# Performance work log

Hardware: AMD Instinct MI355X
Metric: run time of the kernel (lower is better)

## Reference

```python
import jax, jax.numpy as jnp
import numpy as np

TAU = 2.0        # spikingjelly LIFNode default tau
VTH = 1.0        # v_threshold
ALPHA = 2.0      # ATan surrogate alpha
NUM_HEADS = 8
N_WIN = 8
TOPK = 4


@jax.custom_vjp
def atan_heaviside(x):
    # spike = H(v - v_th), with ATan surrogate gradient
    return (x >= 0.0).astype(x.dtype)

def _ah_fwd(x):
    return atan_heaviside(x), x

def _ah_bwd(x, g):
    half_pi_alpha = np.float32(np.pi / 2.0 * ALPHA)
    return (g * (ALPHA / 2.0) / (1.0 + (half_pi_alpha * x) ** 2),)

atan_heaviside.defvjp(_ah_fwd, _ah_bwd)


def lif(x):
    """Multi-step LIF over leading time dim. decay_input=True, v_reset=0, detach_reset."""
    def step(v, xt):
        v = v + (xt - v) / TAU                      # charge
        s = atan_heaviside(v - VTH)                 # fire
        v = v * (1.0 - jax.lax.stop_gradient(s))    # hard reset (detached)
        return v, s
    _, spikes = jax.lax.scan(step, jnp.zeros_like(x[0]), x)
    return spikes


def setup_inputs() -> dict:
    key = jax.random.key(0)
    k1, k2, k3, k4, k5 = jax.random.split(key, 5)
    T, B, L, C = 4, 4, 1024, 256
    x = jax.random.normal(k1, (T, B, L, C), dtype=jnp.float32)
    w_qkv = jax.random.normal(k2, (C, 3 * C), dtype=jnp.float32) * (C ** -0.5)
    b_qkv = jax.random.normal(k3, (3 * C,), dtype=jnp.float32) * 0.02
    w_proj = jax.random.normal(k4, (C, C), dtype=jnp.float32) * (C ** -0.5)
    b_proj = jax.random.normal(k5, (C,), dtype=jnp.float32) * 0.02
    return {"x": x, "w_qkv": w_qkv, "b_qkv": b_qkv, "w_proj": w_proj, "b_proj": b_proj}


def reference(x, w_qkv, b_qkv, w_proj, b_proj):
    T, B, L, C = x.shape
    hd = C // NUM_HEADS
    win = L // N_WIN
    scale = hd ** -0.5

    # --- region-level routing (on raw input summed over time) ---
    xs = x.sum(axis=0).reshape(B, N_WIN, win, C)
    region = xs.sum(axis=2)                                  # [B, n_win, C]
    attn_r = jnp.einsum('bnc,bmc->bnm', region, region) * (C ** -0.5)
    _, idx = jax.lax.top_k(attn_r, TOPK)                     # [B, n_win, topk] int32

    # --- qkv + LIF spiking ---
    qkv = x @ w_qkv + b_qkv                                  # [T,B,L,3C]
    q, k, v = jnp.split(qkv, 3, axis=-1)
    q, k, v = lif(q), lif(k), lif(v)
    q = q.reshape(T, B, N_WIN, win, NUM_HEADS, hd)
    k = k.reshape(T, B, N_WIN, win, NUM_HEADS, hd)
    v = v.reshape(T, B, N_WIN, win, NUM_HEADS, hd)

    # --- gather routed KV windows (vectorized; topk-major concat like torch.cat) ---
    b_idx = jnp.arange(B)[:, None, None]                     # [B,1,1]
    k_g = k[:, b_idx, idx].reshape(T, B, N_WIN, TOPK * win, NUM_HEADS, hd)
    v_g = v[:, b_idx, idx].reshape(T, B, N_WIN, TOPK * win, NUM_HEADS, hd)

    # --- windowed attention over gathered keys ---
    attn = jnp.einsum('tbnqhd,tbnkhd->tbnhqk', q, k_g) * scale
    attn = jax.nn.softmax(attn, axis=-1)
    out = jnp.einsum('tbnhqk,tbnkhd->tbnqhd', attn, v_g).reshape(T, B, L, C)

    out = lif(out @ w_proj + b_proj)
    return out
```

## Files before the change

kernel.cpp:

```cpp
#include <hip/hip_runtime.h>
#include <cstdint>
#include <cstddef>

#define TT 4
#define BB 4
#define LL 1024
#define CC 256
#define HH 8
#define HD 32
#define NWIN 8
#define WIN 128
#define TOPKN 4
#define C3 768

__global__ __launch_bounds__(64) void region_kernel(const float* __restrict__ x,
                                                    float* __restrict__ region) {
    int bn = blockIdx.x;
    int b = bn >> 3, n = bn & 7;
    int c = blockIdx.y * 64 + threadIdx.x;
    float tot = 0.0f;
    for (int r = 0; r < WIN; ++r) {
        int l = n * WIN + r;
        float s = 0.0f;
        for (int t = 0; t < TT; ++t) {
            s += x[(((size_t)t * BB + b) * LL + l) * CC + c];
        }
        tot += s;
    }
    region[(size_t)bn * CC + c] = tot;
}

__global__ __launch_bounds__(64) void route_kernel(const float* __restrict__ region,
                                                   int* __restrict__ idx) {
    int b = blockIdx.x;
    __shared__ float reg[NWIN][CC];
    __shared__ float attn_r[NWIN][NWIN];
    int tid = threadIdx.x;
    for (int e = tid; e < NWIN * CC; e += 64)
        reg[e >> 8][e & 255] = region[(size_t)b * NWIN * CC + e];
    __syncthreads();
    int n = tid >> 3, m = tid & 7;
    float s = 0.0f;
    for (int c = 0; c < CC; ++c) s += reg[n][c] * reg[m][c];
    attn_r[n][m] = s * 0.0625f;
    __syncthreads();
    if (tid < NWIN) {
        float vals[NWIN];
        for (int m2 = 0; m2 < NWIN; ++m2) vals[m2] = attn_r[tid][m2];
        for (int kk = 0; kk < TOPKN; ++kk) {
            int bi = 0; float bv = vals[0];
            for (int m2 = 1; m2 < NWIN; ++m2) {
                if (vals[m2] > bv) { bv = vals[m2]; bi = m2; }
            }
            idx[(b * NWIN + tid) * TOPKN + kk] = bi;
            vals[bi] = -INFINITY;
        }
    }
}

__global__ __launch_bounds__(256, 3) void gemm_bias128(const float* __restrict__ A,
                                                       const float* __restrict__ W,
                                                       const float* __restrict__ bias,
                                                       float* __restrict__ C,
                                                       int M, int N, int K) {
    const int BM = 128, BN = 128, BK = 16, TM = 8;
    __shared__ float As[BK][BM + 4];
    __shared__ float Bs[BK][136];
    int tid = threadIdx.x;
    int tx = tid & 15, ty = tid >> 4;
    int bm = blockIdx.x * BM, bn = blockIdx.y * BN;
    float acc[TM][8] = {};
    for (int k0 = 0; k0 < K; k0 += BK) {
#pragma unroll
        for (int it = 0; it < 2; ++it) {
            int i = it * 256 + tid;
            int row = i >> 2, kc = (i & 3) * 4;
            float4 v = *(const float4*)(A + (size_t)(bm + row) * K + k0 + kc);
            As[kc + 0][row] = v.x; As[kc + 1][row] = v.y;
            As[kc + 2][row] = v.z; As[kc + 3][row] = v.w;
        }
#pragma unroll
        for (int it = 0; it < 2; ++it) {
            int i = it * 256 + tid;
            int kr = i >> 5, nc = (i & 31) * 4;
            float4 v = *(const float4*)(W + (size_t)(k0 + kr) * N + bn + nc);
            *(float4*)&Bs[kr][nc] = v;
        }
        __syncthreads();
#pragma unroll
        for (int kk = 0; kk < BK; ++kk) {
            float a[TM], bb[8];
            const float4* ap = (const float4*)&As[kk][ty * TM];
            float4 a0 = ap[0], a1 = ap[1];
            a[0]=a0.x; a[1]=a0.y; a[2]=a0.z; a[3]=a0.w;
            a[4]=a1.x; a[5]=a1.y; a[6]=a1.z; a[7]=a1.w;
            float4 b0 = *(const float4*)&Bs[kk][tx * 4];
            float4 b1 = *(const float4*)&Bs[kk][64 + tx * 4];
            bb[0]=b0.x; bb[1]=b0.y; bb[2]=b0.z; bb[3]=b0.w;
            bb[4]=b1.x; bb[5]=b1.y; bb[6]=b1.z; bb[7]=b1.w;
#pragma unroll
            for (int i = 0; i < TM; ++i)
#pragma unroll
                for (int j = 0; j < 8; ++j)
                    acc[i][j] = fmaf(a[i], bb[j], acc[i][j]);
        }
        __syncthreads();
    }
#pragma unroll
    for (int i = 0; i < TM; ++i) {
        int row = bm + ty * TM + i;
        int col0 = bn + tx * 4;
        int col1 = bn + 64 + tx * 4;
        float4 o0 = make_float4(acc[i][0] + bias[col0 + 0], acc[i][1] + bias[col0 + 1],
                                acc[i][2] + bias[col0 + 2], acc[i][3] + bias[col0 + 3]);
        float4 o1 = make_float4(acc[i][4] + bias[col1 + 0], acc[i][5] + bias[col1 + 1],
                                acc[i][6] + bias[col1 + 2], acc[i][7] + bias[col1 + 3]);
        *(float4*)&C[(size_t)row * N + col0] = o0;
        *(float4*)&C[(size_t)row * N + col1] = o1;
    }
}

__global__ __launch_bounds__(256, 4) void gemm_bias64(const float* __restrict__ A,
                                                      const float* __restrict__ W,
                                                      const float* __restrict__ bias,
                                                      float* __restrict__ C,
                                                      int M, int N, int K) {
    const int BM = 64, BN = 64, BK = 16;
    __shared__ float As[BK][BM + 4];
    __shared__ float Bs[BK][72];
    int tid = threadIdx.x;
    int tx = tid & 15, ty = tid >> 4;
    int bm = blockIdx.x * BM, bn = blockIdx.y * BN;
    float acc[4][4] = {};
    for (int k0 = 0; k0 < K; k0 += BK) {
        {
            int row = tid >> 2, kc = (tid & 3) * 4;
            float4 v = *(const float4*)(A + (size_t)(bm + row) * K + k0 + kc);
            As[kc + 0][row] = v.x; As[kc + 1][row] = v.y;
            As[kc + 2][row] = v.z; As[kc + 3][row] = v.w;
        }
        {
            int kr = tid >> 4, nc = (tid & 15) * 4;
            float4 v = *(const float4*)(W + (size_t)(k0 + kr) * N + bn + nc);
            *(float4*)&Bs[kr][nc] = v;
        }
        __syncthreads();
#pragma unroll
        for (int kk = 0; kk < BK; ++kk) {
            float4 av = *(const float4*)&As[kk][ty * 4];
            float4 bv = *(const float4*)&Bs[kk][tx * 4];
            float a[4] = {av.x, av.y, av.z, av.w};
            float bb[4] = {bv.x, bv.y, bv.z, bv.w};
#pragma unroll
            for (int i = 0; i < 4; ++i)
#pragma unroll
                for (int j = 0; j < 4; ++j)
                    acc[i][j] = fmaf(a[i], bb[j], acc[i][j]);
        }
        __syncthreads();
    }
#pragma unroll
    for (int i = 0; i < 4; ++i) {
        int row = bm + ty * 4 + i;
        int col = bn + tx * 4;
        float4 o = make_float4(acc[i][0] + bias[col + 0], acc[i][1] + bias[col + 1],
                               acc[i][2] + bias[col + 2], acc[i][3] + bias[col + 3]);
        *(float4*)&C[(size_t)row * N + col] = o;
    }
}

__global__ __launch_bounds__(256) void lif_kernel(const float* src, float* dst, size_t stride) {
    size_t i = ((size_t)blockIdx.x * blockDim.x + threadIdx.x) * 4;
    float v[4] = {0.f, 0.f, 0.f, 0.f};
    for (int t = 0; t < TT; ++t) {
        float4 xv4 = *(const float4*)(src + (size_t)t * stride + i);
        float xv[4] = {xv4.x, xv4.y, xv4.z, xv4.w};
        float sp[4];
#pragma unroll
        for (int j = 0; j < 4; ++j) {
            v[j] = v[j] + (xv[j] - v[j]) * 0.5f;
            bool fire = (v[j] >= 1.0f);
            sp[j] = fire ? 1.0f : 0.0f;
            v[j] = fire ? 0.0f : v[j];
        }
        *(float4*)(dst + (size_t)t * stride + i) = make_float4(sp[0], sp[1], sp[2], sp[3]);
    }
}

__global__ __launch_bounds__(256) void pack_kernel(const float* __restrict__ spk,
                                                   uint32_t* __restrict__ pk) {
    size_t g = (size_t)blockIdx.x * 256 + threadIdx.x;
    int row = (int)(g >> 9);
    int col = (int)(g & 511);
    float v = spk[(size_t)row * C3 + col];
    unsigned long long m = __ballot(v >= 0.5f);
    int lane = threadIdx.x & 63;
    if ((lane & 31) == 0)
        pk[(size_t)row * 16 + (col >> 5)] = (lane < 32) ? (uint32_t)m : (uint32_t)(m >> 32);
}

__global__ __launch_bounds__(256, 4) void attn_fused(const float* __restrict__ spk,
                                                     const uint32_t* __restrict__ pk,
                                                     const int* __restrict__ idxws,
                                                     float* __restrict__ out) {
    int bid = blockIdx.x;
    int h = bid & 1, hp = (bid >> 1) & 3, n = (bid >> 3) & 7, b = (bid >> 6) & 3, t = bid >> 8;
    __shared__ __align__(16) float Vlds[2][64][32];
    __shared__ float ptab[33][WIN];
    __shared__ __align__(16) uint32_t kbs[4 * WIN];
    int tid = threadIdx.x;
    int q = tid & 127, dh = tid >> 7;
    int lbase = (t * BB + b) * LL;

    const int* ip = idxws + (b * NWIN + n) * TOPKN;
    int s0r = ip[0], s1r = ip[1], s2r = ip[2], s3r = ip[3];

#pragma unroll 2
    for (int e = tid; e < 512; e += 256) {
        int w = e >> 7;
        int sw = (w == 0) ? s0r : (w == 1) ? s1r : (w == 2) ? s2r : s3r;
        int row = sw * WIN + (e & 127);
        kbs[e] = pk[(size_t)(lbase + row) * 16 + 8 + hp * 2 + h];
    }
    uint32_t qw = pk[(size_t)(lbase + n * WIN + q) * 16 + hp * 2 + h];
    __syncthreads();

    const float* vsrc = spk + (size_t)lbase * C3 + 512 + hp * 64 + h * 32
                        + (size_t)(tid >> 3) * C3 + (tid & 7) * 4;
    int wvoff = (tid >> 6) * 1024;

#define STAGE_HALF(hw_)                                                              \
    do {                                                                             \
        int hw = (hw_);                                                              \
        int ww = hw >> 1;                                                            \
        int sw = (ww == 0) ? s0r : (ww == 1) ? s1r : (ww == 2) ? s2r : s3r;          \
        const float* src = vsrc + (size_t)sw * (WIN * C3)                            \
                                + (size_t)(hw & 1) * 64 * C3;                        \
        char* lb = (char*)(&Vlds[hw & 1][0][0]) + wvoff;                             \
        __builtin_amdgcn_global_load_lds(                                            \
            (const __attribute__((address_space(1))) void*)src,                      \
            (__attribute__((address_space(3))) void*)lb, 16, 0, 0);                  \
        __builtin_amdgcn_global_load_lds(                                            \
            (const __attribute__((address_space(1))) void*)(src + 32 * C3),          \
            (__attribute__((address_space(3))) void*)(lb + 4096), 16, 0, 0);         \
    } while (0)

    STAGE_HALF(0);
    STAGE_HALF(1);

    const float ALPHA_SC = 0.17677669529663687f;
    const uint4* kb4 = (const uint4*)kbs;
    if (tid < 128) {
        int smax = 0;
#pragma unroll 8
        for (int k4 = 0; k4 < 128; ++k4) {
            uint4 w4 = kb4[k4];
            smax = max(smax, __popc(qw & w4.x));
            smax = max(smax, __popc(qw & w4.y));
            smax = max(smax, __popc(qw & w4.z));
            smax = max(smax, __popc(qw & w4.w));
        }
        float am = __fmul_rn((float)smax, ALPHA_SC);
        float Z = 0.0f;
#pragma unroll 4
        for (int k4 = 0; k4 < 128; ++k4) {
            uint4 w4 = kb4[k4];
            Z += expf(__fsub_rn(__fmul_rn((float)__popc(qw & w4.x), ALPHA_SC), am));
            Z += expf(__fsub_rn(__fmul_rn((float)__popc(qw & w4.y), ALPHA_SC), am));
            Z += expf(__fsub_rn(__fmul_rn((float)__popc(qw & w4.z), ALPHA_SC), am));
            Z += expf(__fsub_rn(__fmul_rn((float)__popc(qw & w4.w), ALPHA_SC), am));
        }
        for (int s = 0; s <= 32; ++s)
            ptab[s][tid] = expf(__fsub_rn(__fmul_rn((float)s, ALPHA_SC), am)) / Z;
    }

    float acc[16];
#pragma unroll
    for (int d = 0; d < 16; ++d) acc[d] = 0.0f;

    asm volatile("s_waitcnt vmcnt(2)" ::: "memory");
    __syncthreads();

#pragma unroll
    for (int hw = 0; hw < 8; ++hw) {
        const uint4* kw4 = kb4 + hw * 16;
        const float* vb = &Vlds[hw & 1][0][dh * 16];
#pragma unroll 2
        for (int g = 0; g < 16; ++g) {
            uint4 kw = kw4[g];
            const float* pr = vb + g * 128;
#pragma unroll
            for (int jp = 0; jp < 2; ++jp) {
                uint32_t ka = (jp == 0) ? kw.x : kw.z;
                uint32_t kb_ = (jp == 0) ? kw.y : kw.w;
                float Pa = ptab[__popc(qw & ka)][q];
                float Pb = ptab[__popc(qw & kb_)][q];
                const float4* va = (const float4*)(pr + jp * 64);
                const float4* vbp = (const float4*)(pr + jp * 64 + 32);
                float4 a0 = va[0], a1 = va[1], a2 = va[2], a3 = va[3];
                float4 b0 = vbp[0], b1 = vbp[1], b2 = vbp[2], b3 = vbp[3];
                acc[ 0] = fmaf(Pa, a0.x, acc[ 0]);
                acc[ 1] = fmaf(Pa, a0.y, acc[ 1]);
                acc[ 2] = fmaf(Pa, a0.z, acc[ 2]);
                acc[ 3] = fmaf(Pa, a0.w, acc[ 3]);
                acc[ 4] = fmaf(Pa, a1.x, acc[ 4]);
                acc[ 5] = fmaf(Pa, a1.y, acc[ 5]);
                acc[ 6] = fmaf(Pa, a1.z, acc[ 6]);
                acc[ 7] = fmaf(Pa, a1.w, acc[ 7]);
                acc[ 8] = fmaf(Pa, a2.x, acc[ 8]);
                acc[ 9] = fmaf(Pa, a2.y, acc[ 9]);
                acc[10] = fmaf(Pa, a2.z, acc[10]);
                acc[11] = fmaf(Pa, a2.w, acc[11]);
                acc[12] = fmaf(Pa, a3.x, acc[12]);
                acc[13] = fmaf(Pa, a3.y, acc[13]);
                acc[14] = fmaf(Pa, a3.z, acc[14]);
                acc[15] = fmaf(Pa, a3.w, acc[15]);
                acc[ 0] = fmaf(Pb, b0.x, acc[ 0]);
                acc[ 1] = fmaf(Pb, b0.y, acc[ 1]);
                acc[ 2] = fmaf(Pb, b0.z, acc[ 2]);
                acc[ 3] = fmaf(Pb, b0.w, acc[ 3]);
                acc[ 4] = fmaf(Pb, b1.x, acc[ 4]);
                acc[ 5] = fmaf(Pb, b1.y, acc[ 5]);
                acc[ 6] = fmaf(Pb, b1.z, acc[ 6]);
                acc[ 7] = fmaf(Pb, b1.w, acc[ 7]);
                acc[ 8] = fmaf(Pb, b2.x, acc[ 8]);
                acc[ 9] = fmaf(Pb, b2.y, acc[ 9]);
                acc[10] = fmaf(Pb, b2.z, acc[10]);
                acc[11] = fmaf(Pb, b2.w, acc[11]);
                acc[12] = fmaf(Pb, b3.x, acc[12]);
                acc[13] = fmaf(Pb, b3.y, acc[13]);
                acc[14] = fmaf(Pb, b3.z, acc[14]);
                acc[15] = fmaf(Pb, b3.w, acc[15]);
            }
        }

        if (hw < 7) {
            __syncthreads();
            if (hw < 6) {
                STAGE_HALF(hw + 2);
                asm volatile("s_waitcnt vmcnt(2)" ::: "memory");
            } else {
                asm volatile("s_waitcnt vmcnt(0)" ::: "memory");
            }
            __syncthreads();
        }
    }
#undef STAGE_HALF

    size_t ob = (size_t)(lbase + n * WIN + q) * CC + (hp * 2 + h) * 32 + dh * 16;
#pragma unroll
    for (int d = 0; d < 16; ++d) out[ob + d] = acc[d];
}

extern "C" void kernel_launch(void* const* d_in, const int* in_sizes, int n_in,
                              void* d_out, int out_size, void* d_ws, size_t ws_size,
                              hipStream_t stream) {
    const float* x      = (const float*)d_in[0];
    const float* w_qkv  = (const float*)d_in[1];
    const float* b_qkv  = (const float*)d_in[2];
    const float* w_proj = (const float*)d_in[3];
    const float* b_proj = (const float*)d_in[4];
    float* ws = (float*)d_ws;

    float* qkv      = ws;
    float* attn_out = ws + 12582912;
    float* proj     = ws + 16777216;
    uint32_t* pkb   = (uint32_t*)proj;
    float* region   = ws + 20971520;
    int*   idxp     = (int*)(ws + 20979712);
    float* outp     = (float*)d_out;

    region_kernel<<<dim3(BB * NWIN, 4), dim3(64), 0, stream>>>(x, region);
    route_kernel<<<dim3(BB), dim3(64), 0, stream>>>(region, idxp);
    gemm_bias128<<<dim3(128, 6), dim3(256), 0, stream>>>(x, w_qkv, b_qkv, qkv,
                                                         TT * BB * LL, C3, CC);
    lif_kernel<<<dim3(3072), dim3(256), 0, stream>>>(qkv, qkv, (size_t)BB * LL * C3);
    pack_kernel<<<dim3(32768), dim3(256), 0, stream>>>(qkv, pkb);
    attn_fused<<<dim3(TT * BB * NWIN * 4 * 2), dim3(256), 0, stream>>>(qkv, pkb, idxp, attn_out);
    gemm_bias64<<<dim3(256, 4), dim3(256), 0, stream>>>(attn_out, w_proj, b_proj, proj,
                                                        TT * BB * LL, CC, CC);
    lif_kernel<<<dim3(1024), dim3(256), 0, stream>>>(proj, outp, (size_t)BB * LL * CC);
}
```

Before: 280.9 us.

## Fuse LIF with bit packing and split softmax stats from PV attention

Replaces the separate LIF and pack kernels with one kernel that runs LIF over time, writes float spikes only for V, and packs q/k spikes into bitmasks via ballots. Softmax max and normalizer computation moves to a separate attn_sm kernel, so the PV kernel no longer has half its threads idle during the stats pass. The PV kernel now computes two queries per thread over 8 dims each to reuse V LDS loads, and stores with vector writes. This adds one kernel launch and a small workspace buffer, and uses a permuted bit order inside the packed words that stays consistent between q and k.

```diff
diff --git a/kernel.cpp b/kernel.cpp
--- a/kernel.cpp
+++ b/kernel.cpp
@@ -187,29 +187,105 @@
     }
 }
 
-__global__ __launch_bounds__(256) void pack_kernel(const float* __restrict__ spk,
-                                                   uint32_t* __restrict__ pk) {
-    size_t g = (size_t)blockIdx.x * 256 + threadIdx.x;
-    int row = (int)(g >> 9);
-    int col = (int)(g & 511);
-    float v = spk[(size_t)row * C3 + col];
-    unsigned long long m = __ballot(v >= 0.5f);
-    int lane = threadIdx.x & 63;
-    if ((lane & 31) == 0)
-        pk[(size_t)row * 16 + (col >> 5)] = (lane < 32) ? (uint32_t)m : (uint32_t)(m >> 32);
-}
-
-__global__ __launch_bounds__(256, 4) void attn_fused(const float* __restrict__ spk,
-                                                     const uint32_t* __restrict__ pk,
-                                                     const int* __restrict__ idxws,
-                                                     float* __restrict__ out) {
+__global__ __launch_bounds__(192) void lif_pack_kernel(float* __restrict__ qkv,
+                                                       uint32_t* __restrict__ pk) {
+    int row = blockIdx.x;
+    int tid = threadIdx.x;
+    int c = tid * 4;
+    int wid = tid >> 6;
+    int lane = tid & 63;
+    const size_t stride = (size_t)BB * LL * C3;
+    float* base = qkv + (size_t)row * C3 + c;
+
+    float v[4] = {0.f, 0.f, 0.f, 0.f};
+    for (int t = 0; t < TT; ++t) {
+        float4 xv4 = *(const float4*)(base + (size_t)t * stride);
+        float xv[4] = {xv4.x, xv4.y, xv4.z, xv4.w};
+        bool fire[4];
+        float sp[4];
+#pragma unroll
+        for (int j = 0; j < 4; ++j) {
+            v[j] = v[j] + (xv[j] - v[j]) * 0.5f;
+            fire[j] = (v[j] >= 1.0f);
+            sp[j] = fire[j] ? 1.0f : 0.0f;
+            v[j] = fire[j] ? 0.0f : v[j];
+        }
+        if (c >= 512)
+            *(float4*)(base + (size_t)t * stride) = make_float4(sp[0], sp[1], sp[2], sp[3]);
+        unsigned long long B0 = __ballot(fire[0]);
+        unsigned long long B1 = __ballot(fire[1]);
+        unsigned long long B2 = __ballot(fire[2]);
+        unsigned long long B3 = __ballot(fire[3]);
+        if (lane < 8 && wid < 2) {
+            uint32_t word = ((uint32_t)(B0 >> (8 * lane)) & 0xFFu)
+                          | (((uint32_t)(B1 >> (8 * lane)) & 0xFFu) << 8)
+                          | (((uint32_t)(B2 >> (8 * lane)) & 0xFFu) << 16)
+                          | (((uint32_t)(B3 >> (8 * lane)) & 0xFFu) << 24);
+            pk[((size_t)t * BB * LL + row) * 16 + wid * 8 + lane] = word;
+        }
+    }
+}
+
+__global__ __launch_bounds__(256) void attn_sm(const uint32_t* __restrict__ pk,
+                                               const int* __restrict__ idxws,
+                                               float2* __restrict__ amz) {
+    int bid = blockIdx.x;
+    int hp = bid & 3, n = (bid >> 2) & 7, b = (bid >> 5) & 3, t = bid >> 7;
+    __shared__ uint32_t kbs[2][512];
+    int tid = threadIdx.x;
+    int q = tid & 127, h = tid >> 7;
+    int lbase = (t * BB + b) * LL;
+
+    const int* ip = idxws + (b * NWIN + n) * TOPKN;
+    int s0r = ip[0], s1r = ip[1], s2r = ip[2], s3r = ip[3];
+
+#pragma unroll 4
+    for (int e = tid; e < 1024; e += 256) {
+        int hh = e >> 9, kk = e & 511;
+        int w = kk >> 7;
+        int sw = (w == 0) ? s0r : (w == 1) ? s1r : (w == 2) ? s2r : s3r;
+        int row = sw * WIN + (kk & 127);
+        kbs[hh][kk] = pk[(size_t)(lbase + row) * 16 + 8 + hp * 2 + hh];
+    }
+    uint32_t qw = pk[(size_t)(lbase + n * WIN + q) * 16 + hp * 2 + h];
+    __syncthreads();
+
+    const float ALPHA_SC = 0.17677669529663687f;
+    const uint4* kb4 = (const uint4*)kbs[h];
+    int smax = 0;
+#pragma unroll 8
+    for (int k4 = 0; k4 < 128; ++k4) {
+        uint4 w4 = kb4[k4];
+        smax = max(smax, __popc(qw & w4.x));
+        smax = max(smax, __popc(qw & w4.y));
+        smax = max(smax, __popc(qw & w4.z));
+        smax = max(smax, __popc(qw & w4.w));
+    }
+    float am = __fmul_rn((float)smax, ALPHA_SC);
+    float Z = 0.0f;
+#pragma unroll 4
+    for (int k4 = 0; k4 < 128; ++k4) {
+        uint4 w4 = kb4[k4];
+        Z += expf(__fsub_rn(__fmul_rn((float)__popc(qw & w4.x), ALPHA_SC), am));
+        Z += expf(__fsub_rn(__fmul_rn((float)__popc(qw & w4.y), ALPHA_SC), am));
+        Z += expf(__fsub_rn(__fmul_rn((float)__popc(qw & w4.z), ALPHA_SC), am));
+        Z += expf(__fsub_rn(__fmul_rn((float)__popc(qw & w4.w), ALPHA_SC), am));
+    }
+    amz[(size_t)(lbase + n * WIN + q) * HH + hp * 2 + h] = make_float2(am, Z);
+}
+
+__global__ __launch_bounds__(256, 4) void attn_pv(const float* __restrict__ spk,
+                                                  const uint32_t* __restrict__ pk,
+                                                  const int* __restrict__ idxws,
+                                                  const float2* __restrict__ amz,
+                                                  float* __restrict__ out) {
     int bid = blockIdx.x;
     int h = bid & 1, hp = (bid >> 1) & 3, n = (bid >> 3) & 7, b = (bid >> 6) & 3, t = bid >> 8;
     __shared__ __align__(16) float Vlds[2][64][32];
     __shared__ float ptab[33][WIN];
     __shared__ __align__(16) uint32_t kbs[4 * WIN];
     int tid = threadIdx.x;
-    int q = tid & 127, dh = tid >> 7;
+    int qg = tid & 63, dh = tid >> 6;
     int lbase = (t * BB + b) * LL;
 
     const int* ip = idxws + (b * NWIN + n) * TOPKN;
@@ -222,8 +298,8 @@
         int row = sw * WIN + (e & 127);
         kbs[e] = pk[(size_t)(lbase + row) * 16 + 8 + hp * 2 + h];
     }
-    uint32_t qw = pk[(size_t)(lbase + n * WIN + q) * 16 + hp * 2 + h];
-    __syncthreads();
+    uint32_t qw0 = pk[(size_t)(lbase + n * WIN + qg) * 16 + hp * 2 + h];
+    uint32_t qw1 = pk[(size_t)(lbase + n * WIN + qg + 64) * 16 + hp * 2 + h];
 
     const float* vsrc = spk + (size_t)lbase * C3 + 512 + hp * 64 + h * 32
                         + (size_t)(tid >> 3) * C3 + (tid & 7) * 4;
@@ -248,43 +324,28 @@
     STAGE_HALF(0);
     STAGE_HALF(1);
 
-    const float ALPHA_SC = 0.17677669529663687f;
-    const uint4* kb4 = (const uint4*)kbs;
-    if (tid < 128) {
-        int smax = 0;
-#pragma unroll 8
-        for (int k4 = 0; k4 < 128; ++k4) {
-            uint4 w4 = kb4[k4];
-            smax = max(smax, __popc(qw & w4.x));
-            smax = max(smax, __popc(qw & w4.y));
-            smax = max(smax, __popc(qw & w4.z));
-            smax = max(smax, __popc(qw & w4.w));
-        }
-        float am = __fmul_rn((float)smax, ALPHA_SC);
-        float Z = 0.0f;
-#pragma unroll 4
-        for (int k4 = 0; k4 < 128; ++k4) {
-            uint4 w4 = kb4[k4];
-            Z += expf(__fsub_rn(__fmul_rn((float)__popc(qw & w4.x), ALPHA_SC), am));
-            Z += expf(__fsub_rn(__fmul_rn((float)__popc(qw & w4.y), ALPHA_SC), am));
-            Z += expf(__fsub_rn(__fmul_rn((float)__popc(qw & w4.z), ALPHA_SC), am));
-            Z += expf(__fsub_rn(__fmul_rn((float)__popc(qw & w4.w), ALPHA_SC), am));
-        }
-        for (int s = 0; s <= 32; ++s)
-            ptab[s][tid] = expf(__fsub_rn(__fmul_rn((float)s, ALPHA_SC), am)) / Z;
-    }
-
-    float acc[16];
-#pragma unroll
-    for (int d = 0; d < 16; ++d) acc[d] = 0.0f;
+    {
+        if (tid < 128) {
+            float2 az = amz[(size_t)(lbase + n * WIN + tid) * HH + hp * 2 + h];
+            const float ALPHA_SC = 0.17677669529663687f;
+            for (int s = 0; s <= 32; ++s)
+                ptab[s][tid] = expf(__fsub_rn(__fmul_rn((float)s, ALPHA_SC), az.x)) / az.y;
+        }
+    }
+
+    float acc0[8], acc1[8];
+#pragma unroll
+    for (int d = 0; d < 8; ++d) { acc0[d] = 0.0f; acc1[d] = 0.0f; }
 
     asm volatile("s_waitcnt vmcnt(2)" ::: "memory");
     __syncthreads();
 
+    const uint4* kb4 = (const uint4*)kbs;
+
 #pragma unroll
     for (int hw = 0; hw < 8; ++hw) {
         const uint4* kw4 = kb4 + hw * 16;
-        const float* vb = &Vlds[hw & 1][0][dh * 16];
+        const float* vb = &Vlds[hw & 1][0][dh * 8];
 #pragma unroll 2
         for (int g = 0; g < 16; ++g) {
             uint4 kw = kw4[g];
@@ -293,44 +354,30 @@
             for (int jp = 0; jp < 2; ++jp) {
                 uint32_t ka = (jp == 0) ? kw.x : kw.z;
                 uint32_t kb_ = (jp == 0) ? kw.y : kw.w;
-                float Pa = ptab[__popc(qw & ka)][q];
-                float Pb = ptab[__popc(qw & kb_)][q];
+                float Pa0 = ptab[__popc(qw0 & ka)][qg];
+                float Pa1 = ptab[__popc(qw1 & ka)][qg + 64];
+                float Pb0 = ptab[__popc(qw0 & kb_)][qg];
+                float Pb1 = ptab[__popc(qw1 & kb_)][qg + 64];
                 const float4* va = (const float4*)(pr + jp * 64);
                 const float4* vbp = (const float4*)(pr + jp * 64 + 32);
-                float4 a0 = va[0], a1 = va[1], a2 = va[2], a3 = va[3];
-                float4 b0 = vbp[0], b1 = vbp[1], b2 = vbp[2], b3 = vbp[3];
-                acc[ 0] = fmaf(Pa, a0.x, acc[ 0]);
-                acc[ 1] = fmaf(Pa, a0.y, acc[ 1]);
-                acc[ 2] = fmaf(Pa, a0.z, acc[ 2]);
-                acc[ 3] = fmaf(Pa, a0.w, acc[ 3]);
-                acc[ 4] = fmaf(Pa, a1.x, acc[ 4]);
-                acc[ 5] = fmaf(Pa, a1.y, acc[ 5]);
-                acc[ 6] = fmaf(Pa, a1.z, acc[ 6]);
-                acc[ 7] = fmaf(Pa, a1.w, acc[ 7]);
-                acc[ 8] = fmaf(Pa, a2.x, acc[ 8]);
-                acc[ 9] = fmaf(Pa, a2.y, acc[ 9]);
-                acc[10] = fmaf(Pa, a2.z, acc[10]);
-                acc[11] = fmaf(Pa, a2.w, acc[11]);
-                acc[12] = fmaf(Pa, a3.x, acc[12]);
-                acc[13] = fmaf(Pa, a3.y, acc[13]);
-                acc[14] = fmaf(Pa, a3.z, acc[14]);
-                acc[15] = fmaf(Pa, a3.w, acc[15]);
-                acc[ 0] = fmaf(Pb, b0.x, acc[ 0]);
-                acc[ 1] = fmaf(Pb, b0.y, acc[ 1]);
-                acc[ 2] = fmaf(Pb, b0.z, acc[ 2]);
-                acc[ 3] = fmaf(Pb, b0.w, acc[ 3]);
-                acc[ 4] = fmaf(Pb, b1.x, acc[ 4]);
-                acc[ 5] = fmaf(Pb, b1.y, acc[ 5]);
-                acc[ 6] = fmaf(Pb, b1.z, acc[ 6]);
-                acc[ 7] = fmaf(Pb, b1.w, acc[ 7]);
-                acc[ 8] = fmaf(Pb, b2.x, acc[ 8]);
-                acc[ 9] = fmaf(Pb, b2.y, acc[ 9]);
-                acc[10] = fmaf(Pb, b2.z, acc[10]);
-                acc[11] = fmaf(Pb, b2.w, acc[11]);
-                acc[12] = fmaf(Pb, b3.x, acc[12]);
-                acc[13] = fmaf(Pb, b3.y, acc[13]);
-                acc[14] = fmaf(Pb, b3.z, acc[14]);
-                acc[15] = fmaf(Pb, b3.w, acc[15]);
+                float4 a0 = va[0], a1 = va[1];
+                float4 b0 = vbp[0], b1 = vbp[1];
+                acc0[0] = fmaf(Pa0, a0.x, acc0[0]);  acc1[0] = fmaf(Pa1, a0.x, acc1[0]);
+                acc0[1] = fmaf(Pa0, a0.y, acc0[1]);  acc1[1] = fmaf(Pa1, a0.y, acc1[1]);
+                acc0[2] = fmaf(Pa0, a0.z, acc0[2]);  acc1[2] = fmaf(Pa1, a0.z, acc1[2]);
+                acc0[3] = fmaf(Pa0, a0.w, acc0[3]);  acc1[3] = fmaf(Pa1, a0.w, acc1[3]);
+                acc0[4] = fmaf(Pa0, a1.x, acc0[4]);  acc1[4] = fmaf(Pa1, a1.x, acc1[4]);
+                acc0[5] = fmaf(Pa0, a1.y, acc0[5]);  acc1[5] = fmaf(Pa1, a1.y, acc1[5]);
+                acc0[6] = fmaf(Pa0, a1.z, acc0[6]);  acc1[6] = fmaf(Pa1, a1.z, acc1[6]);
+                acc0[7] = fmaf(Pa0, a1.w, acc0[7]);  acc1[7] = fmaf(Pa1, a1.w, acc1[7]);
+                acc0[0] = fmaf(Pb0, b0.x, acc0[0]);  acc1[0] = fmaf(Pb1, b0.x, acc1[0]);
+                acc0[1] = fmaf(Pb0, b0.y, acc0[1]);  acc1[1] = fmaf(Pb1, b0.y, acc1[1]);
+                acc0[2] = fmaf(Pb0, b0.z, acc0[2]);  acc1[2] = fmaf(Pb1, b0.z, acc1[2]);
+                acc0[3] = fmaf(Pb0, b0.w, acc0[3]);  acc1[3] = fmaf(Pb1, b0.w, acc1[3]);
+                acc0[4] = fmaf(Pb0, b1.x, acc0[4]);  acc1[4] = fmaf(Pb1, b1.x, acc1[4]);
+                acc0[5] = fmaf(Pb0, b1.y, acc0[5]);  acc1[5] = fmaf(Pb1, b1.y, acc1[5]);
+                acc0[6] = fmaf(Pb0, b1.z, acc0[6]);  acc1[6] = fmaf(Pb1, b1.z, acc1[6]);
+                acc0[7] = fmaf(Pb0, b1.w, acc0[7]);  acc1[7] = fmaf(Pb1, b1.w, acc1[7]);
             }
         }
 
@@ -347,9 +394,12 @@
     }
 #undef STAGE_HALF
 
-    size_t ob = (size_t)(lbase + n * WIN + q) * CC + (hp * 2 + h) * 32 + dh * 16;
-#pragma unroll
-    for (int d = 0; d < 16; ++d) out[ob + d] = acc[d];
+    size_t ob0 = (size_t)(lbase + n * WIN + qg) * CC + (hp * 2 + h) * 32 + dh * 8;
+    size_t ob1 = ob0 + (size_t)64 * CC;
+    *(float4*)&out[ob0]     = make_float4(acc0[0], acc0[1], acc0[2], acc0[3]);
+    *(float4*)&out[ob0 + 4] = make_float4(acc0[4], acc0[5], acc0[6], acc0[7]);
+    *(float4*)&out[ob1]     = make_float4(acc1[0], acc1[1], acc1[2], acc1[3]);
+    *(float4*)&out[ob1 + 4] = make_float4(acc1[4], acc1[5], acc1[6], acc1[7]);
 }
 
 extern "C" void kernel_launch(void* const* d_in, const int* in_sizes, int n_in,
@@ -368,15 +418,16 @@
     uint32_t* pkb   = (uint32_t*)proj;
     float* region   = ws + 20971520;
     int*   idxp     = (int*)(ws + 20979712);
+    float2* amzp    = (float2*)(ws + 20979840);
     float* outp     = (float*)d_out;
 
     region_kernel<<<dim3(BB * NWIN, 4), dim3(64), 0, stream>>>(x, region);
     route_kernel<<<dim3(BB), dim3(64), 0, stream>>>(region, idxp);
     gemm_bias128<<<dim3(128, 6), dim3(256), 0, stream>>>(x, w_qkv, b_qkv, qkv,
                                                          TT * BB * LL, C3, CC);
-    lif_kernel<<<dim3(3072), dim3(256), 0, stream>>>(qkv, qkv, (size_t)BB * LL * C3);
-    pack_kernel<<<dim3(32768), dim3(256), 0, stream>>>(qkv, pkb);
-    attn_fused<<<dim3(TT * BB * NWIN * 4 * 2), dim3(256), 0, stream>>>(qkv, pkb, idxp, attn_out);
+    lif_pack_kernel<<<dim3(BB * LL), dim3(192), 0, stream>>>(qkv, pkb);
+    attn_sm<<<dim3(TT * BB * NWIN * 4), dim3(256), 0, stream>>>(pkb, idxp, amzp);
+    attn_pv<<<dim3(TT * BB * NWIN * 4 * 2), dim3(256), 0, stream>>>(qkv, pkb, idxp, amzp, attn_out);
     gemm_bias64<<<dim3(256, 4), dim3(256), 0, stream>>>(attn_out, w_proj, b_proj, proj,
                                                         TT * BB * LL, CC, CC);
     lif_kernel<<<dim3(1024), dim3(256), 0, stream>>>(proj, outp, (size_t)BB * LL * CC);
```

New measurement: 261.4 us. -6.9%, faster.
